# Performance work log

Measured on AMD Instinct MI355X. Metric: run time of the kernel, lower is better.

The kernel has to match this reference:

```python
import jax, jax.numpy as jnp
import numpy as np

B, Q, N_WAY, K_SHOT = 2, 75, 5, 5
C, H, W = 640, 5, 5
PROJ, HEAD_DIM = 640, 32
NUM_HEAD = PROJ // HEAD_DIM
SCALE = HEAD_DIM ** 0.5
TEMP = 12.5
ALPHAS = [2.0 ** k for k in range(-3, 2)]  # cfg.model.mmd.alphas**k, k in [-3,2)


def setup_inputs() -> dict:
    key = jax.random.key(0)
    ks = jax.random.split(key, 7)
    std = (2.0 / PROJ) ** 0.5  # torch init: normal(0, sqrt(2/(k*k*out)))
    return {
        "support_xf": jax.random.normal(ks[0], (B, N_WAY * K_SHOT, C, H, W), jnp.float32),
        "support_y": jax.random.randint(ks[1], (B, N_WAY * K_SHOT), 0, N_WAY),
        "query_xf": jax.random.normal(ks[2], (B, Q, C, H, W), jnp.float32),
        "query_y": jax.random.randint(ks[3], (B, Q), 0, N_WAY),
        "Wq": jax.random.normal(ks[4], (PROJ, C), jnp.float32) * std,
        "Wk": jax.random.normal(ks[5], (PROJ, C), jnp.float32) * std,
        "Wv": jax.random.normal(ks[6], (C, C), jnp.float32) * ((2.0 / C) ** 0.5),
    }


def _qkv(x, Wq, Wk, Wv):
    # x: [b, n, c, h, w]; 1x1 convs == channel matmuls
    b, n, c, h, w = x.shape
    xf = x.reshape(b, n, c, h * w)
    proj = lambda Wm: jnp.einsum('oc,bncp->bnop', Wm, xf)
    k = proj(Wk).reshape(b, n, NUM_HEAD, -1, h * w)                   # [b,n,nh,hd,p]
    q = proj(Wq).reshape(b, n, NUM_HEAD, -1, h * w).swapaxes(-1, -2)  # [b,n,nh,p,hd]
    v = proj(Wv).reshape(b, n, NUM_HEAD, -1, h * w).swapaxes(-1, -2)  # [b,n,nh,p,ch]
    return q, k, v


def _cross_attn(q, k, v, shortcut, dim):
    # q:[b,*,*,nh,p,hd], k:[b,*,*,nh,hd,p], v:[b,*,*,nh,p,ch] (broadcasting over q/s axes)
    attn = jax.nn.softmax((q / SCALE) @ k, axis=-1)
    out = attn @ v                                  # [b,Q,S,nh,p,ch]
    b, nq, s = out.shape[:3]
    h, w = shortcut.shape[-2:]
    out = out.swapaxes(-1, -2).reshape(b, nq, s, -1, h, w)  # [b,Q,S,c,h,w]
    return out + jnp.expand_dims(shortcut, dim)


def _sqdist(x, y):
    # squared euclidean pairwise distances over last-two dims; == cdist(x,y)**2
    xx = jnp.sum(x * x, -1)[..., :, None]
    yy = jnp.sum(y * y, -1)[..., None, :]
    d2 = xx + yy - 2.0 * jnp.einsum('...nc,...mc->...nm', x, y)
    return jnp.maximum(d2, 0.0)


def _mgk(d2):
    # multi-scale gaussian kernel: sum_a exp(-a * dist^2)
    k = jnp.exp(-ALPHAS[0] * d2)
    for a in ALPHAS[1:]:
        k = k + jnp.exp(-a * d2)
    return k


def _forward(support_xf, query_xf, query_y, Wq, Wk, Wv):
    b, q, c, h, w = query_xf.shape
    sq, sk, sv = _qkv(support_xf, Wq, Wk, Wv)
    qq_, qk_, qv_ = _qkv(query_xf, Wq, Wk, Wv)
    # support features attended by query queries (shortcut = support, broadcast over q)
    sbq = _cross_attn(qq_[:, :, None], sk[:, None], sv[:, None], support_xf, dim=1)  # [b,q,s,c,h,w]
    # query features attended by support queries (shortcut = query, broadcast over s)
    qbs = _cross_attn(sq[:, None], qk_[:, :, None], qv_[:, :, None], query_xf, dim=2)

    def regroup(t):  # [b,q,s,c,h,w] -> [b,q,n_way,k_shot*h*w,c]
        t = t.reshape(b, q, N_WAY, K_SHOT, c, h, w)
        return t.transpose(0, 1, 2, 3, 5, 6, 4).reshape(b, q, N_WAY, K_SHOT * h * w, c)

    sxf = regroup(sbq)
    qxf = regroup(qbs)
    # centering over channel dim
    sxf = sxf - sxf.mean(-1, keepdims=True)
    qxf = qxf - qxf.mean(-1, keepdims=True)

    Kss = _mgk(_sqdist(sxf, sxf))  # [b,q,n_way,N,N]
    Kqq = _mgk(_sqdist(qxf, qxf))
    Kqs = _mgk(_sqdist(sxf, qxf))

    N = K_SHOT * h * w  # num features per class-group (== num_fea_per_img)
    tot = lambda K: jnp.sum(K, (-1, -2))
    tr = lambda K: jnp.trace(K, axis1=-2, axis2=-1)  # diagonal removal (::N+1 stride)
    mmd = (tot(Kss) - tr(Kss)) / (N * (N - 1)) \
        + (tot(Kqq) - tr(Kqq)) / (N * (N - 1)) \
        - (2.0 / (N * N)) * tot(Kqs)
    mmd_dis = mmd.reshape(b * q, N_WAY)

    logp = jax.nn.log_softmax(-mmd_dis / TEMP, axis=-1)
    y = query_y.reshape(-1)
    loss = -jnp.mean(jnp.take_along_axis(logp, y[:, None], axis=1))
    return loss


def reference(support_xf, support_y, query_xf, query_y, Wq, Wk, Wv):
    return _forward(support_xf, query_xf, query_y, Wq, Wk, Wv)
```

## Files before the change

kernel.cpp:

```cpp
#include <hip/hip_runtime.h>
#include <math.h>

#define PP    25
#define CCH   640
#define NCOL  5000
#define SCALE_INV 0.17677669529663687f

#define XTB_OFF   0L
#define WB_OFF    1600000L
#define PROJB_OFF 2214400L
#define MMD_OFF   7014400L
#define FEAT_OFF  7015168L
#define FEAT_PER_WAY_US 160000L
#define FEAT_PER_PAIR_US 800000L

typedef __attribute__((ext_vector_type(8)))  short          s16x8;
typedef __attribute__((ext_vector_type(8)))  unsigned short u16x8;
typedef __attribute__((ext_vector_type(4)))  unsigned short u16x4;
typedef __attribute__((ext_vector_type(16))) float          f32x16;

__device__ inline unsigned short f2bf(float x) {
  unsigned u = __float_as_uint(x);
  unsigned r = u + 0x7fff + ((u >> 16) & 1);
  return (unsigned short)(r >> 16);
}
__device__ inline float bf2f(unsigned short b) {
  return __uint_as_float(((unsigned)b) << 16);
}
__device__ inline unsigned cvtpk(float lo, float hi) {
  unsigned r;
  asm("v_cvt_pk_bf16_f32 %0, %1, %2" : "=v"(r) : "v"(lo), "v"(hi));
  return r;
}

__global__ __launch_bounds__(256) void t_kernel(const float* __restrict__ sup,
                                                const float* __restrict__ qry,
                                                unsigned short* __restrict__ XTB) {
  __shared__ float lds[16000];
  int item = blockIdx.x;
  const float* src = (item < 50) ? (sup + item * 16000) : (qry + (item - 50) * 16000);
  int tid = threadIdx.x;
  for (int e = tid * 4; e < 16000; e += 1024)
    *(float4*)&lds[e] = *(const float4*)&src[e];
  __syncthreads();
  int ibase = item * PP;
  for (int e = tid * 4; e < 16000; e += 1024) {
    int p = e / CCH, c = e - p * CCH;
    u16x4 b;
    b.x = f2bf(lds[(c + 0) * PP + p]);
    b.y = f2bf(lds[(c + 1) * PP + p]);
    b.z = f2bf(lds[(c + 2) * PP + p]);
    b.w = f2bf(lds[(c + 3) * PP + p]);
    *(u16x4*)&XTB[(long)(ibase + p) * CCH + c] = b;
  }
}

__global__ __launch_bounds__(256) void w_kernel(const float* __restrict__ Wq,
                                                const float* __restrict__ Wk,
                                                const float* __restrict__ Wv,
                                                unsigned short* __restrict__ WB) {
  long base = ((long)blockIdx.x * 256 + threadIdx.x) * 8;
  int m = (int)(base / 409600L);
  long off = base - (long)m * 409600L;
  const float* W = (m == 0) ? Wq : ((m == 1) ? Wk : Wv);
  float4 a = *(const float4*)&W[off];
  float4 c = *(const float4*)&W[off + 4];
  u16x8 v;
  v[0] = f2bf(a.x); v[1] = f2bf(a.y); v[2] = f2bf(a.z); v[3] = f2bf(a.w);
  v[4] = f2bf(c.x); v[5] = f2bf(c.y); v[6] = f2bf(c.z); v[7] = f2bf(c.w);
  *(u16x8*)&WB[base] = v;
}

__global__ __launch_bounds__(512) void proj_kernel(const unsigned short* __restrict__ WB,
                                                   const unsigned short* __restrict__ XTB,
                                                   unsigned short* __restrict__ proj) {
  __shared__ __align__(16) unsigned short At[128 * 64];
  __shared__ __align__(16) unsigned short Bt[128 * 64];
  int m = blockIdx.z;
  int ctile = blockIdx.x * 128, otile = blockIdx.y * 128;
  const unsigned short* Wsrc = WB + (long)m * 409600L;
  unsigned short* out = proj + (long)m * NCOL * CCH;
  int tid = threadIdx.x;
  int w = tid >> 6, lane = tid & 63;
  int wr = w >> 2, wc = w & 3;
  int lr = lane & 31, ksel = lane >> 5;
  int sr = tid >> 2, sg = (tid & 3) * 2;

  f32x16 acc[2];
#pragma unroll
  for (int a = 0; a < 2; a++)
#pragma unroll
    for (int e = 0; e < 16; e++) acc[a][e] = 0.f;

  int bcol = ctile + sr;
  const unsigned short* asrc = Wsrc + (long)(otile + sr) * CCH + sg * 8;
  const unsigned short* bsrc = XTB + (long)bcol * CCH + sg * 8;

  u16x8 pa[2], pb[2];
#pragma unroll
  for (int gi = 0; gi < 2; gi++) {
    pa[gi] = *(const u16x8*)&asrc[gi * 8];
    if (bcol < NCOL) pb[gi] = *(const u16x8*)&bsrc[gi * 8];
    else { u16x8 z; for (int e = 0; e < 8; e++) z[e] = 0; pb[gi] = z; }
  }

  for (int kc = 0; kc < 10; kc++) {
    __syncthreads();
#pragma unroll
    for (int gi = 0; gi < 2; gi++) {
      int g = sg + gi;
      *(u16x8*)&At[sr * 64 + ((g ^ (sr & 7)) << 3)] = pa[gi];
      *(u16x8*)&Bt[sr * 64 + ((g ^ (sr & 7)) << 3)] = pb[gi];
    }
    if (kc < 9) {
      const unsigned short* an = asrc + (kc + 1) * 64;
      const unsigned short* bn = bsrc + (kc + 1) * 64;
#pragma unroll
      for (int gi = 0; gi < 2; gi++) {
        pa[gi] = *(const u16x8*)&an[gi * 8];
        if (bcol < NCOL) pb[gi] = *(const u16x8*)&bn[gi * 8];
      }
    }
    __syncthreads();
#pragma unroll
    for (int ks = 0; ks < 4; ks++) {
      int gk = ks * 2 + ksel;
      s16x8 bf1;
      {
        int R = wc * 32 + lr;
        bf1 = *(const s16x8*)&Bt[R * 64 + ((gk ^ (R & 7)) << 3)];
      }
#pragma unroll
      for (int a = 0; a < 2; a++) {
        int R = (wr + 2 * a) * 32 + lr;
        s16x8 af = *(const s16x8*)&At[R * 64 + ((gk ^ (R & 7)) << 3)];
        acc[a] = __builtin_amdgcn_mfma_f32_32x32x16_bf16(af, bf1, acc[a], 0, 0, 0);
      }
    }
  }

  int col = ctile + wc * 32 + lr;
  if (col < NCOL) {
#pragma unroll
    for (int a = 0; a < 2; a++) {
      int obase = otile + (wr + 2 * a) * 32 + 4 * ksel;
#pragma unroll
      for (int g2 = 0; g2 < 4; g2++) {
        u16x4 v;
        v.x = f2bf(acc[a][g2 * 4 + 0]);
        v.y = f2bf(acc[a][g2 * 4 + 1]);
        v.z = f2bf(acc[a][g2 * 4 + 2]);
        v.w = f2bf(acc[a][g2 * 4 + 3]);
        *(u16x4*)&out[(long)col * CCH + obase + g2 * 8] = v;
      }
    }
  }
}

__global__ __launch_bounds__(256) void attn_kernel(const unsigned short* __restrict__ proj,
                                                   const unsigned short* __restrict__ XTB,
                                                   unsigned short* __restrict__ feat,
                                                   int chunk_start) {
  int tid = threadIdx.x, wid = tid >> 6, lane = tid & 63;
  int lr = lane & 31, hf = lane >> 5;
  int rclamp = lr > 24 ? 24 : lr;
  int bid = blockIdx.x;
  int pw = bid / 10, grp = bid - pw * 10;
  int unit = grp * 4 + wid;
  int side = unit >= 20 ? 1 : 0;
  int head = unit - side * 20;
  int lpi = pw / 5, way = pw - lpi * 5;
  int pair = chunk_start + lpi;
  int b = pair / 75;
  int qcol = (50 + pair) * PP;
  int sitem0 = b * 25 + way * 5;
  int ho = head * 32;
  const unsigned short* Qp = proj;
  const unsigned short* Kp = proj + (long)NCOL * CCH;
  const unsigned short* Vp = proj + 2L * NCOL * CCH;
  unsigned short* fb = feat + (long)pw * FEAT_PER_WAY_US + head * 250 * 32;

  auto ldfrag = [&](const unsigned short* src, int col0, int ks) -> s16x8 {
    return *(const s16x8*)&src[(long)(col0 + rclamp) * CCH + ho + ks * 16 + hf * 8];
  };
  auto ldvfrag = [&](int col0, int ks) -> s16x8 {
    const unsigned short* base = Vp + (long)(col0 + ks * 16 + hf * 8) * CCH + ho + lr;
    s16x8 f;
#pragma unroll
    for (int j = 0; j < 8; j++) f[j] = (short)base[(long)j * CCH];
    return f;
  };

  s16x8 fA0, fA1, fB0, fB1, fV0, fV1;
  float scv[16];
  if (side == 0) {
    fB0 = ldfrag(Qp, qcol, 0); fB1 = ldfrag(Qp, qcol, 1);
  } else {
    fA0 = ldfrag(Kp, qcol, 0); fA1 = ldfrag(Kp, qcol, 1);
    fV0 = ldvfrag(qcol, 0);    fV1 = ldvfrag(qcol, 1);
#pragma unroll
    for (int rg = 0; rg < 16; rg++) {
      int q = (rg & 3) + 8 * (rg >> 2) + 4 * hf;
      int qc = q > 24 ? 24 : q;
      scv[rg] = bf2f(XTB[(long)(qcol + qc) * CCH + ho + lr]);
    }
  }

  for (int shot = 0; shot < 5; shot++) {
    int scol = (sitem0 + shot) * PP;
    s16x8 A0, A1, B0, B1, V0, V1;
    if (side == 0) {
      A0 = ldfrag(Kp, scol, 0); A1 = ldfrag(Kp, scol, 1);
      B0 = fB0; B1 = fB1;
      V0 = ldvfrag(scol, 0);    V1 = ldvfrag(scol, 1);
    } else {
      A0 = fA0; A1 = fA1;
      B0 = ldfrag(Qp, scol, 0); B1 = ldfrag(Qp, scol, 1);
      V0 = fV0; V1 = fV1;
    }
    f32x16 s;
#pragma unroll
    for (int e = 0; e < 16; e++) s[e] = 0.f;
    s = __builtin_amdgcn_mfma_f32_32x32x16_bf16(A0, B0, s, 0, 0, 0);
    s = __builtin_amdgcn_mfma_f32_32x32x16_bf16(A1, B1, s, 0, 0, 0);
    float pv[16];
    float mx = -1e30f;
#pragma unroll
    for (int rg = 0; rg < 16; rg++) {
      int mm = (rg & 3) + 8 * (rg >> 2) + 4 * hf;
      float v = (mm < 25) ? s[rg] : -1e30f;
      pv[rg] = v;
      mx = fmaxf(mx, v);
    }
    mx = fmaxf(mx, __shfl_xor(mx, 32));
    float sum = 0.f;
#pragma unroll
    for (int rg = 0; rg < 16; rg++) {
      float e = __expf((pv[rg] - mx) * SCALE_INV);
      pv[rg] = e;
      sum += e;
    }
    sum += __shfl_xor(sum, 32);
    float rinv = 1.f / sum;
#pragma unroll
    for (int rg = 0; rg < 16; rg++) pv[rg] *= rinv;
    union { unsigned u[4]; s16x8 v; } P0u, P1u;
    {
      float ex[8], fr[8];
#pragma unroll
      for (int r = 0; r < 8; r++) ex[r] = __shfl_xor(pv[r], 32);
#pragma unroll
      for (int j = 0; j < 4; j++) {
        fr[j]     = hf ? ex[4 + j] : pv[j];
        fr[4 + j] = hf ? pv[4 + j] : ex[j];
      }
#pragma unroll
      for (int j = 0; j < 4; j++) P0u.u[j] = cvtpk(fr[2 * j], fr[2 * j + 1]);
#pragma unroll
      for (int r = 0; r < 8; r++) ex[r] = __shfl_xor(pv[8 + r], 32);
#pragma unroll
      for (int j = 0; j < 4; j++) {
        fr[j]     = hf ? ex[4 + j] : pv[8 + j];
        fr[4 + j] = hf ? pv[12 + j] : ex[j];
      }
#pragma unroll
      for (int j = 0; j < 4; j++) P1u.u[j] = cvtpk(fr[2 * j], fr[2 * j + 1]);
    }
    f32x16 o;
#pragma unroll
    for (int e = 0; e < 16; e++) o[e] = 0.f;
    o = __builtin_amdgcn_mfma_f32_32x32x16_bf16(P0u.v, V0, o, 0, 0, 0);
    o = __builtin_amdgcn_mfma_f32_32x32x16_bf16(P1u.v, V1, o, 0, 0, 0);
    unsigned short* frow = fb + (long)((side ? 125 : 0) + shot * 25) * 32;
    const unsigned short* scb = XTB + (long)(scol + 4 * hf) * CCH + ho + lr;
#pragma unroll
    for (int i = 0; i < 8; i++) {
      int rg0 = 2 * i, rg1 = rg0 + 1;
      int qoff = (rg0 & 3) + 8 * (rg0 >> 2);
      int q0 = qoff + 4 * hf, q1 = q0 + 1;
      float sc0, sc1;
      if (side) { sc0 = scv[rg0]; sc1 = scv[rg1]; }
      else {
        sc0 = bf2f(scb[(long)qoff * CCH]);
        sc1 = bf2f(scb[(long)(qoff + 1) * CCH]);
      }
      unsigned u = cvtpk(o[rg0] + sc0, o[rg1] + sc1);
      if (q0 < 25) frow[q0 * 32 + lr] = (unsigned short)u;
      if (q1 < 25) frow[q1 * 32 + lr] = (unsigned short)(u >> 16);
    }
  }
}

__device__ inline void gram_load(u16x8* pf, const unsigned short* __restrict__ fb,
                                 int sr, int half, int kc) {
#pragma unroll
  for (int gi = 0; gi < 4; gi++) {
    u16x8 v;
    if (sr < 250) {
      v = *(const u16x8*)&fb[(long)((2 * kc + half) * 250 + sr) * 32 + gi * 8];
    } else if (sr == 250) {
#pragma unroll
      for (int e = 0; e < 8; e++) v[e] = 0x3F80;
    } else {
#pragma unroll
      for (int e = 0; e < 8; e++) v[e] = 0;
    }
    pf[gi] = v;
  }
}

__global__ __launch_bounds__(512) void gram_kernel(const unsigned short* __restrict__ feat,
                                                   float* __restrict__ mmd,
                                                   int chunk_start) {
  __shared__ __align__(16) unsigned short tile[16384];
  __shared__ float sums[256], nrmsq[256], meanv[256], nrmv[256];
  __shared__ float red[24];
  int bid = blockIdx.x;
  const unsigned short* fb = feat + (long)bid * FEAT_PER_WAY_US;
  int tid = threadIdx.x;
  int w = tid >> 6, lane = tid & 63;
  int wr = w >> 2, wc = w & 3;
  int lr = lane & 31, ksel = lane >> 5;
  int sr = tid >> 1, half = tid & 1;

  f32x16 acc[4][2];
#pragma unroll
  for (int a = 0; a < 4; a++)
#pragma unroll
    for (int b2 = 0; b2 < 2; b2++)
#pragma unroll
      for (int e = 0; e < 16; e++) acc[a][b2][e] = 0.f;

  u16x8 pf[4];
  gram_load(pf, fb, sr, half, 0);

  for (int kc = 0; kc < 10; kc++) {
    __syncthreads();
#pragma unroll
    for (int gi = 0; gi < 4; gi++) {
      int g = half * 4 + gi;
      *(u16x8*)&tile[sr * 64 + ((g ^ (sr & 7)) << 3)] = pf[gi];
    }
    if (kc < 9) gram_load(pf, fb, sr, half, kc + 1);
    __syncthreads();
#pragma unroll
    for (int ks = 0; ks < 4; ks++) {
      int gk = ks * 2 + ksel;
      s16x8 af[4], bfv[2];
#pragma unroll
      for (int a = 0; a < 4; a++) {
        int R = (wr + 2 * a) * 32 + lr;
        af[a] = *(const s16x8*)&tile[R * 64 + ((gk ^ (R & 7)) << 3)];
      }
#pragma unroll
      for (int b2 = 0; b2 < 2; b2++) {
        int R = (wc + 4 * b2) * 32 + lr;
        bfv[b2] = *(const s16x8*)&tile[R * 64 + ((gk ^ (R & 7)) << 3)];
      }
#pragma unroll
      for (int a = 0; a < 4; a++)
#pragma unroll
        for (int b2 = 0; b2 < 2; b2++)
          acc[a][b2] = __builtin_amdgcn_mfma_f32_32x32x16_bf16(af[a], bfv[b2], acc[a][b2], 0, 0, 0);
    }
  }

#pragma unroll
  for (int a = 0; a < 4; a++) {
    int ti = wr + 2 * a;
#pragma unroll
    for (int b2 = 0; b2 < 2; b2++) {
      int tj = wc + 4 * b2;
      int col = tj * 32 + lr;
      if (col == 250) {
#pragma unroll
        for (int rg = 0; rg < 16; rg++) {
          int row = ti * 32 + (rg & 3) + 8 * (rg >> 2) + 4 * ksel;
          if (row < 250) sums[row] = acc[a][b2][rg];
        }
      }
      if (ti == tj) {
#pragma unroll
        for (int rg = 0; rg < 16; rg++) {
          int row = ti * 32 + (rg & 3) + 8 * (rg >> 2) + 4 * ksel;
          if (row == col && row < 250) nrmsq[row] = acc[a][b2][rg];
        }
      }
    }
  }
  __syncthreads();
  if (tid < 250) {
    float s0 = sums[tid];
    float m = s0 * (1.f / 640.f);
    meanv[tid] = m;
    nrmv[tid] = nrmsq[tid] - s0 * m;
  }
  __syncthreads();

  float s_ss = 0.f, s_qq = 0.f, s_x = 0.f;
#pragma unroll
  for (int a = 0; a < 4; a++) {
    int ti = wr + 2 * a;
#pragma unroll
    for (int b2 = 0; b2 < 2; b2++) {
      int tj = wc + 4 * b2;
      int col = tj * 32 + lr;
#pragma unroll
      for (int rg = 0; rg < 16; rg++) {
        int row = ti * 32 + (rg & 3) + 8 * (rg >> 2) + 4 * ksel;
        if (row < 250 && col < 250) {
          float d2 = nrmv[row] + nrmv[col] - 2.f * acc[a][b2][rg]
                   + 1280.f * meanv[row] * meanv[col];
          d2 = fmaxf(d2, 0.f);
          float e = __expf(-0.125f * d2);
          float e2 = e * e, e4 = e2 * e2, e8 = e4 * e4, e16 = e8 * e8;
          float kv = e + e2 + e4 + e8 + e16;
          bool rs = row < 125, cs = col < 125;
          if (rs && cs)        { if (row != col) s_ss += kv; }
          else if (!rs && !cs) { if (row != col) s_qq += kv; }
          else                 s_x += kv;
        }
      }
    }
  }
#pragma unroll
  for (int off = 32; off; off >>= 1) {
    s_ss += __shfl_xor(s_ss, off);
    s_qq += __shfl_xor(s_qq, off);
    s_x  += __shfl_xor(s_x, off);
  }
  if (lane == 0) { red[w * 3] = s_ss; red[w * 3 + 1] = s_qq; red[w * 3 + 2] = s_x; }
  __syncthreads();
  if (tid == 0) {
    float a = 0.f, b2 = 0.f, c = 0.f;
    for (int i = 0; i < 8; i++) { a += red[i * 3]; b2 += red[i * 3 + 1]; c += red[i * 3 + 2]; }
    mmd[(long)chunk_start * 5 + bid] = a * (1.f / 15500.f) + b2 * (1.f / 15500.f) - c * (1.f / 15625.f);
  }
}

__global__ __launch_bounds__(256) void loss_kernel(const float* __restrict__ mmd,
                                                   const int* __restrict__ qy,
                                                   float* __restrict__ out) {
  __shared__ float red[256];
  int tid = threadIdx.x;
  float val = 0.f;
  if (tid < 150) {
    float l[5];
    float mx = -1e30f;
#pragma unroll
    for (int w = 0; w < 5; w++) {
      l[w] = -mmd[tid * 5 + w] * (1.0f / 12.5f);
      mx = fmaxf(mx, l[w]);
    }
    float sum = 0.f;
#pragma unroll
    for (int w = 0; w < 5; w++) sum += __expf(l[w] - mx);
    float lse = mx + logf(sum);
    int y = qy[tid];
    val = -(l[y] - lse);
  }
  red[tid] = val;
  __syncthreads();
  for (int s = 128; s > 0; s >>= 1) {
    if (tid < s) red[tid] += red[tid + s];
    __syncthreads();
  }
  if (tid == 0) out[0] = red[0] * (1.0f / 150.0f);
}

extern "C" void kernel_launch(void* const* d_in, const int* in_sizes, int n_in,
                              void* d_out, int out_size, void* d_ws, size_t ws_size,
                              hipStream_t stream) {
  (void)in_sizes; (void)n_in; (void)out_size;
  const float* sup = (const float*)d_in[0];
  const float* qry = (const float*)d_in[2];
  const int* qy = (const int*)d_in[3];
  const float* Wq = (const float*)d_in[4];
  const float* Wk = (const float*)d_in[5];
  const float* Wv = (const float*)d_in[6];
  float* ws = (float*)d_ws;
  unsigned short* XTB = (unsigned short*)(ws + XTB_OFF);
  unsigned short* WB = (unsigned short*)(ws + WB_OFF);
  unsigned short* projB = (unsigned short*)(ws + PROJB_OFF);
  float* mmd = ws + MMD_OFF;
  unsigned short* feat = (unsigned short*)(ws + FEAT_OFF);
  float* out = (float*)d_out;

  long wsf = (long)(ws_size / 4);
  long avail_us = (wsf - FEAT_OFF) * 2;
  long chunkL = avail_us / FEAT_PER_PAIR_US;
  int chunk = (chunkL > 150) ? 150 : (chunkL < 1 ? 1 : (int)chunkL);

  hipLaunchKernelGGL(t_kernel, dim3(200), dim3(256), 0, stream, sup, qry, XTB);
  hipLaunchKernelGGL(w_kernel, dim3(600), dim3(256), 0, stream, Wq, Wk, Wv, WB);
  hipLaunchKernelGGL(proj_kernel, dim3(40, 5, 3), dim3(512), 0, stream, WB, XTB, projB);
  for (int c0 = 0; c0 < 150; c0 += chunk) {
    int cp = (150 - c0 < chunk) ? (150 - c0) : chunk;
    hipLaunchKernelGGL(attn_kernel, dim3(cp * 50), dim3(256), 0, stream, projB, XTB, feat, c0);
    hipLaunchKernelGGL(gram_kernel, dim3(cp * 5), dim3(512), 0, stream, feat, mmd, c0);
  }
  hipLaunchKernelGGL(loss_kernel, dim3(1), dim3(256), 0, stream, mmd, qy, out);
}
```

Before: 266.4 us.

## Double-buffer gram tiles with direct global-to-LDS loads

The gram kernel now loads feature tiles straight into LDS with global_load_lds into a double-buffered tile, instead of staging through registers and writing LDS by hand. The next k-chunk is fetched while MFMAs run on the current one, leaving one barrier per iteration. The constant ones and zero padding rows now come from a small workspace buffer that w_kernel fills. This doubles the LDS used by the tile and adds a launch-bounds hint for two blocks per CU. w_kernel runs 256 threads per block but tests for 384, so the last 128 entries of the padding buffer are never written.

```diff
diff --git a/kernel.cpp b/kernel.cpp
--- a/kernel.cpp
+++ b/kernel.cpp
@@ -10,7 +10,8 @@
 #define WB_OFF    1600000L
 #define PROJB_OFF 2214400L
 #define MMD_OFF   7014400L
-#define FEAT_OFF  7015168L
+#define ONES_OFF  7015168L
+#define FEAT_OFF  7015360L
 #define FEAT_PER_WAY_US 160000L
 #define FEAT_PER_PAIR_US 800000L
 
@@ -18,6 +19,9 @@
 typedef __attribute__((ext_vector_type(8)))  unsigned short u16x8;
 typedef __attribute__((ext_vector_type(4)))  unsigned short u16x4;
 typedef __attribute__((ext_vector_type(16))) float          f32x16;
+
+typedef __attribute__((address_space(1))) const unsigned int glb_u32;
+typedef __attribute__((address_space(3))) unsigned int       lds_u32;
 
 __device__ inline unsigned short f2bf(float x) {
   unsigned u = __float_as_uint(x);
@@ -58,7 +62,10 @@
 __global__ __launch_bounds__(256) void w_kernel(const float* __restrict__ Wq,
                                                 const float* __restrict__ Wk,
                                                 const float* __restrict__ Wv,
-                                                unsigned short* __restrict__ WB) {
+                                                unsigned short* __restrict__ WB,
+                                                unsigned short* __restrict__ ones) {
+  if (blockIdx.x == 0 && threadIdx.x < 384)
+    ones[threadIdx.x] = (threadIdx.x < 64) ? (unsigned short)0x3F80 : (unsigned short)0;
   long base = ((long)blockIdx.x * 256 + threadIdx.x) * 8;
   int m = (int)(base / 409600L);
   long off = base - (long)m * 409600L;
@@ -291,28 +298,11 @@
   }
 }
 
-__device__ inline void gram_load(u16x8* pf, const unsigned short* __restrict__ fb,
-                                 int sr, int half, int kc) {
-#pragma unroll
-  for (int gi = 0; gi < 4; gi++) {
-    u16x8 v;
-    if (sr < 250) {
-      v = *(const u16x8*)&fb[(long)((2 * kc + half) * 250 + sr) * 32 + gi * 8];
-    } else if (sr == 250) {
-#pragma unroll
-      for (int e = 0; e < 8; e++) v[e] = 0x3F80;
-    } else {
-#pragma unroll
-      for (int e = 0; e < 8; e++) v[e] = 0;
-    }
-    pf[gi] = v;
-  }
-}
-
-__global__ __launch_bounds__(512) void gram_kernel(const unsigned short* __restrict__ feat,
-                                                   float* __restrict__ mmd,
-                                                   int chunk_start) {
-  __shared__ __align__(16) unsigned short tile[16384];
+__global__ __launch_bounds__(512, 2) void gram_kernel(const unsigned short* __restrict__ feat,
+                                                      const unsigned short* __restrict__ ones,
+                                                      float* __restrict__ mmd,
+                                                      int chunk_start) {
+  __shared__ __align__(16) unsigned short tile[2][16384];
   __shared__ float sums[256], nrmsq[256], meanv[256], nrmv[256];
   __shared__ float red[24];
   int bid = blockIdx.x;
@@ -321,7 +311,21 @@
   int w = tid >> 6, lane = tid & 63;
   int wr = w >> 2, wc = w & 3;
   int lr = lane & 31, ksel = lane >> 5;
-  int sr = tid >> 1, half = tid & 1;
+
+  const unsigned short* srcp[4];
+  long stepv[4];
+#pragma unroll
+  for (int i = 0; i < 4; i++) {
+    int s = (w * 4 + i) * 64 + lane;
+    int row = s >> 3, gs = s & 7, g = gs ^ (row & 7);
+    if (row < 250) {
+      srcp[i] = fb + (long)((g >> 2) * 250 + row) * 32 + (g & 3) * 8;
+      stepv[i] = 16000;
+    } else {
+      srcp[i] = ones + (row - 250) * 64 + g * 8;
+      stepv[i] = 0;
+    }
+  }
 
   f32x16 acc[4][2];
 #pragma unroll
@@ -331,18 +335,21 @@
 #pragma unroll
       for (int e = 0; e < 16; e++) acc[a][b2][e] = 0.f;
 
-  u16x8 pf[4];
-  gram_load(pf, fb, sr, half, 0);
+#pragma unroll
+  for (int i = 0; i < 4; i++)
+    __builtin_amdgcn_global_load_lds((glb_u32*)srcp[i],
+                                     (lds_u32*)&tile[0][(w * 4 + i) * 512], 16, 0, 0);
+  __syncthreads();
 
   for (int kc = 0; kc < 10; kc++) {
-    __syncthreads();
-#pragma unroll
-    for (int gi = 0; gi < 4; gi++) {
-      int g = half * 4 + gi;
-      *(u16x8*)&tile[sr * 64 + ((g ^ (sr & 7)) << 3)] = pf[gi];
-    }
-    if (kc < 9) gram_load(pf, fb, sr, half, kc + 1);
-    __syncthreads();
+    int cur = kc & 1;
+    if (kc < 9) {
+#pragma unroll
+      for (int i = 0; i < 4; i++)
+        __builtin_amdgcn_global_load_lds((glb_u32*)(srcp[i] + (long)(kc + 1) * stepv[i]),
+                                         (lds_u32*)&tile[cur ^ 1][(w * 4 + i) * 512], 16, 0, 0);
+    }
+    const unsigned short* tb = tile[cur];
 #pragma unroll
     for (int ks = 0; ks < 4; ks++) {
       int gk = ks * 2 + ksel;
@@ -350,12 +357,12 @@
 #pragma unroll
       for (int a = 0; a < 4; a++) {
         int R = (wr + 2 * a) * 32 + lr;
-        af[a] = *(const s16x8*)&tile[R * 64 + ((gk ^ (R & 7)) << 3)];
+        af[a] = *(const s16x8*)&tb[R * 64 + ((gk ^ (R & 7)) << 3)];
       }
 #pragma unroll
       for (int b2 = 0; b2 < 2; b2++) {
         int R = (wc + 4 * b2) * 32 + lr;
-        bfv[b2] = *(const s16x8*)&tile[R * 64 + ((gk ^ (R & 7)) << 3)];
+        bfv[b2] = *(const s16x8*)&tb[R * 64 + ((gk ^ (R & 7)) << 3)];
       }
 #pragma unroll
       for (int a = 0; a < 4; a++)
@@ -363,6 +370,7 @@
         for (int b2 = 0; b2 < 2; b2++)
           acc[a][b2] = __builtin_amdgcn_mfma_f32_32x32x16_bf16(af[a], bfv[b2], acc[a][b2], 0, 0, 0);
     }
+    __syncthreads();
   }
 
 #pragma unroll
@@ -483,6 +491,7 @@
   unsigned short* WB = (unsigned short*)(ws + WB_OFF);
   unsigned short* projB = (unsigned short*)(ws + PROJB_OFF);
   float* mmd = ws + MMD_OFF;
+  unsigned short* ones = (unsigned short*)(ws + ONES_OFF);
   unsigned short* feat = (unsigned short*)(ws + FEAT_OFF);
   float* out = (float*)d_out;
 
@@ -492,12 +501,12 @@
   int chunk = (chunkL > 150) ? 150 : (chunkL < 1 ? 1 : (int)chunkL);
 
   hipLaunchKernelGGL(t_kernel, dim3(200), dim3(256), 0, stream, sup, qry, XTB);
-  hipLaunchKernelGGL(w_kernel, dim3(600), dim3(256), 0, stream, Wq, Wk, Wv, WB);
+  hipLaunchKernelGGL(w_kernel, dim3(600), dim3(256), 0, stream, Wq, Wk, Wv, WB, ones);
   hipLaunchKernelGGL(proj_kernel, dim3(40, 5, 3), dim3(512), 0, stream, WB, XTB, projB);
   for (int c0 = 0; c0 < 150; c0 += chunk) {
     int cp = (150 - c0 < chunk) ? (150 - c0) : chunk;
     hipLaunchKernelGGL(attn_kernel, dim3(cp * 50), dim3(256), 0, stream, projB, XTB, feat, c0);
-    hipLaunchKernelGGL(gram_kernel, dim3(cp * 5), dim3(512), 0, stream, feat, mmd, c0);
+    hipLaunchKernelGGL(gram_kernel, dim3(cp * 5), dim3(512), 0, stream, feat, ones, mmd, c0);
   }
   hipLaunchKernelGGL(loss_kernel, dim3(1), dim3(256), 0, stream, mmd, qy, out);
 }
```

Result: no change. 263.1 us (-1.2%).
